# Optimization experiments

Hardware: AMD Instinct MI355X
Metric: run time of the kernel (lower is better)

Reference implementation:

```python
import jax, jax.numpy as jnp
import numpy as np

K = 8           # neighbor_num
H = 8           # n_heads
DH = 64         # dim_single_head


def setup_inputs() -> dict:
    key = jax.random.key(0)
    ks = jax.random.split(key, 6)
    B, N, D = 2, 8192, 256
    inner = H * DH  # 512
    x = jax.random.normal(ks[0], (B, N, D), jnp.float32)
    center_pos3d = jax.random.normal(ks[1], (B, N, 3), jnp.float32)
    Wq = jax.random.normal(ks[2], (D, inner), jnp.float32) * 0.02
    Wkv = jax.random.normal(ks[3], (D, 2 * inner), jnp.float32) * 0.02
    Wout = jax.random.normal(ks[4], (inner, D), jnp.float32) * 0.02
    bout = jnp.zeros((D,), jnp.float32)
    return {"x": x, "center_pos3d": center_pos3d, "Wq": Wq, "Wkv": Wkv,
            "Wout": Wout, "bout": bout}


def _knn_idx(pos, k):
    # pos: [B,N,3] -> indices of k nearest neighbors per point, [B,N,k]
    sq = jnp.sum(pos * pos, axis=-1)                      # [B,N]
    d2 = sq[:, :, None] + sq[:, None, :] - 2.0 * jnp.einsum('bnc,bmc->bnm', pos, pos)
    _, idx = jax.lax.top_k(-d2, k)                        # smallest distances
    return idx


def reference(x, center_pos3d, Wq, Wkv, Wout, bout):
    B, N, D = x.shape
    inner = H * DH
    scale = DH ** -0.5

    idx = _knn_idx(center_pos3d, K)                       # [B,N,K] int32
    # grouping_operation: gather neighbor features -> [B,N,K,D]
    knn_x = jax.vmap(lambda xb, ib: xb[ib])(x, idx)

    q = (x @ Wq).reshape(B, N, H, DH)                     # [B,N,H,DH]
    kv = knn_x @ Wkv                                      # [B,N,K,2*inner]
    k_, v_ = jnp.split(kv, 2, axis=-1)
    k_ = k_.reshape(B, N, K, H, DH)
    v_ = v_.reshape(B, N, K, H, DH)

    dots = jnp.einsum('bnhd,bnkhd->bnhk', q, k_) * scale  # [B,N,H,K]
    attn = jax.nn.softmax(dots, axis=-1)
    out = jnp.einsum('bnhk,bnkhd->bnhd', attn, v_)        # [B,N,H,DH]
    out = out.reshape(B, N, inner)
    return out @ Wout + bout                              # dropout p=0 -> identity
```

## Files before the change

kernel.cpp:

```cpp
#include <hip/hip_runtime.h>
#include <hip/hip_bf16.h>

#define N_PTS 8192
#define KNN 8

typedef __attribute__((ext_vector_type(8))) short short8;
typedef __attribute__((ext_vector_type(4))) float float4v;
typedef unsigned long long u64;

static __device__ __forceinline__ short f2bf(float f) {
    unsigned u = __float_as_uint(f);
    unsigned r = (u + 0x7FFFu + ((u >> 16) & 1u)) >> 16;
    return (short)r;
}
static __device__ __forceinline__ float bf2f(short s) {
    return __uint_as_float(((unsigned)(unsigned short)s) << 16);
}

static __device__ __forceinline__ unsigned sortkey(float f) {
    unsigned u = __float_as_uint(f);
    return u ^ (((unsigned)((int)u >> 31)) | 0x80000000u);
}

static __device__ __forceinline__ void ins8(u64* best, u64 x) {
#pragma unroll
    for (int j = 0; j < 8; ++j) {
        const u64 lo = x < best[j] ? x : best[j];
        const u64 hi = x < best[j] ? best[j] : x;
        best[j] = lo; x = hi;
    }
}

static __device__ __forceinline__ void vmin_acc(float& acc, float d) {
    asm("v_min_f32 %0, %0, %1" : "+v"(acc) : "v"(d));
}
static __device__ __forceinline__ void vsort2(float& a, float& x) {
    float lo, hi;
    asm("v_min_f32 %0, %2, %3\n\tv_max_f32 %1, %2, %3"
        : "=&v"(lo), "=v"(hi) : "v"(a), "v"(x));
    a = lo; x = hi;
}

__global__ __launch_bounds__(256) void fused_knn_conv(const float* __restrict__ pos,
                                                      u64* __restrict__ partial,
                                                      const float* __restrict__ x,
                                                      const float* __restrict__ Wq,
                                                      const float* __restrict__ Wkv,
                                                      const float* __restrict__ Wout,
                                                      short* __restrict__ xb,
                                                      short* __restrict__ wqkvt,
                                                      short* __restrict__ woutt)
{
    __shared__ __align__(16) char smem[16896];
    const int tid = threadIdx.x;
    const int g5 = blockIdx.x / 5;
    const int r5 = blockIdx.x % 5;

    if (r5 == 0) {
        const int kb = g5;
        float4* cand = (float4*)smem;
        unsigned short* buf = (unsigned short*)(smem + 8192);

        const int p   = kb & 15;
        const int qg  = kb >> 4;
        const int batch = qg >> 5;
        const int q_in_b = (qg & 31) * 256 + tid;
        const float* bpos = pos + (long)batch * N_PTS * 3;

        if (tid < 128) {
            const float* src = bpos + (p * 512 + tid * 4) * 3;
            const float4 f0 = *(const float4*)(src);
            const float4 f1 = *(const float4*)(src + 4);
            const float4 f2 = *(const float4*)(src + 8);
            const int c0 = tid * 4;
            cand[c0 + 0] = make_float4(f0.x, f0.y, f0.z,
                                       fmaf(f0.x, f0.x, fmaf(f0.y, f0.y, f0.z * f0.z)));
            cand[c0 + 1] = make_float4(f0.w, f1.x, f1.y,
                                       fmaf(f0.w, f0.w, fmaf(f1.x, f1.x, f1.y * f1.y)));
            cand[c0 + 2] = make_float4(f1.z, f1.w, f2.x,
                                       fmaf(f1.z, f1.z, fmaf(f1.w, f1.w, f2.x * f2.x)));
            cand[c0 + 3] = make_float4(f2.y, f2.z, f2.w,
                                       fmaf(f2.y, f2.y, fmaf(f2.z, f2.z, f2.w * f2.w)));
        }
        __syncthreads();

        const float qx = bpos[q_in_b * 3 + 0];
        const float qy = bpos[q_in_b * 3 + 1];
        const float qz = bpos[q_in_b * 3 + 2];
        const float nqx = -2.0f * qx;
        const float nqy = -2.0f * qy;
        const float nqz = -2.0f * qz;

        float bmin[32];
#pragma unroll
        for (int j = 0; j < 32; ++j) bmin[j] = 3.0e38f;

        for (int base = 0; base < 512; base += 32) {
#pragma unroll
            for (int g = 0; g < 32; ++g) {
                const float4 c = cand[base + g];
                const float d = fmaf(c.x, nqx, fmaf(c.y, nqy, fmaf(c.z, nqz, c.w)));
                vmin_acc(bmin[g], d);
            }
        }

        float t8[8];
#pragma unroll
        for (int j = 0; j < 8; ++j) t8[j] = 3.0e38f;
#pragma unroll
        for (int i = 0; i < 32; ++i) {
            float x_ = bmin[i];
#pragma unroll
            for (int j = 0; j < 8; ++j)
                vsort2(t8[j], x_);
        }
        const float t = t8[7];

        int cnt = 0;
        for (int base = 0; base < 512; base += 32) {
#pragma unroll
            for (int g = 0; g < 32; ++g) {
                const float4 c = cand[base + g];
                const float d = fmaf(c.x, nqx, fmaf(c.y, nqy, fmaf(c.z, nqz, c.w)));
                if (d <= t) {
                    buf[tid * 17 + (cnt < 16 ? cnt : 16)] = (unsigned short)(base + g);
                    ++cnt;
                }
            }
        }

        u64 best[8];
#pragma unroll
        for (int j = 0; j < 8; ++j) best[j] = ~0ULL;

        if (cnt <= 16) {
            for (int u = 0; u < cnt; ++u) {
                const int i = buf[tid * 17 + u];
                const float4 c = cand[i];
                const float d = fmaf(c.x, nqx, fmaf(c.y, nqy, fmaf(c.z, nqz, c.w)));
                ins8(best, ((u64)sortkey(d) << 32) | (unsigned)(p * 512 + i));
            }
        } else {
            for (int i = 0; i < 512; ++i) {
                const float4 c = cand[i];
                const float d = fmaf(c.x, nqx, fmaf(c.y, nqy, fmaf(c.z, nqz, c.w)));
                const u64 x_ = ((u64)sortkey(d) << 32) | (unsigned)(p * 512 + i);
                if (x_ < best[7]) ins8(best, x_);
            }
        }

        const long qglob = (long)batch * N_PTS + q_in_b;
#pragma unroll
        for (int j = 0; j < 8; ++j)
            partial[(long)(p * 8 + j) * 16384 + qglob] = best[j];

    } else {
        const int bid = g5 * 4 + (r5 - 1);
        if (bid < 2048) {
            const int i = bid * 256 + tid;
            const float4 a = ((const float4*)x)[i * 2];
            const float4 b = ((const float4*)x)[i * 2 + 1];
            short8 w = {f2bf(a.x), f2bf(a.y), f2bf(a.z), f2bf(a.w),
                        f2bf(b.x), f2bf(b.y), f2bf(b.z), f2bf(b.w)};
            ((short8*)xb)[i] = w;
        } else if (bid < 2560) {
            const int o = (bid - 2048) * 256 + tid;
            const int n = o >> 8, k = o & 255;
            wqkvt[o] = f2bf(Wq[(long)k * 512 + n]);
        } else if (bid < 3584) {
            const int o = (bid - 2560) * 256 + tid;
            const int n = o >> 8, k = o & 255;
            wqkvt[131072 + o] = f2bf(Wkv[(long)k * 1024 + n]);
        } else {
            const int o = (bid - 3584) * 256 + tid;
            const int n = o >> 9, k = o & 511;
            woutt[o] = f2bf(Wout[(long)k * 256 + n]);
        }
    }
}

__global__ __launch_bounds__(256) void fused_gemm_merge(const short* __restrict__ A,
                                                        const short* __restrict__ Bt,
                                                        short* __restrict__ qall,
                                                        short* __restrict__ kvall,
                                                        const u64* __restrict__ partial,
                                                        int* __restrict__ idxo)
{
    __shared__ short As[128][40];
    __shared__ short Bs[128][40];

    const int tid = threadIdx.x;

    if (blockIdx.x < 64) {
        const int q = blockIdx.x * 256 + tid;
        u64 best[8];
#pragma unroll
        for (int j = 0; j < 8; ++j) best[j] = ~0ULL;
        for (int s = 0; s < 128; ++s) {
            u64 x = partial[(long)s * 16384 + q];
            if (x < best[7]) ins8(best, x);
        }
#pragma unroll
        for (int j = 0; j < 8; ++j)
            idxo[(long)q * 8 + j] = (int)(best[j] & 0xFFFFFFFFu);
        return;
    }

    const int id = blockIdx.x - 64;
    const int bx = id % 12;
    const int by = id / 12;

    const int lane = tid & 63;
    const int wv   = tid >> 6;
    const int quad = lane >> 4;
    const int l15  = lane & 15;
    const int m0 = by * 128;
    const int n0 = bx * 128;
    const int mh = (wv & 1) * 64, nh = (wv >> 1) * 64;

    const int srow  = tid >> 1;
    const int shalf = (tid & 1) * 16;
    const int Kd = 256;

    float4v acc[4][4];
#pragma unroll
    for (int i = 0; i < 4; ++i)
#pragma unroll
        for (int j = 0; j < 4; ++j) acc[i][j] = (float4v)(0.f);

    for (int k0 = 0; k0 < Kd; k0 += 32) {
        const short8* asrc = (const short8*)(A + (long)(m0 + srow) * Kd + k0 + shalf);
        const short8* bsrc = (const short8*)(Bt + (long)(n0 + srow) * Kd + k0 + shalf);
        *(short8*)&As[srow][shalf]     = asrc[0];
        *(short8*)&As[srow][shalf + 8] = asrc[1];
        *(short8*)&Bs[srow][shalf]     = bsrc[0];
        *(short8*)&Bs[srow][shalf + 8] = bsrc[1];
        __syncthreads();

        short8 af[4], bfv[4];
#pragma unroll
        for (int i = 0; i < 4; ++i)
            af[i] = *(const short8*)&As[mh + i * 16 + l15][quad * 8];
#pragma unroll
        for (int j = 0; j < 4; ++j)
            bfv[j] = *(const short8*)&Bs[nh + j * 16 + l15][quad * 8];
#pragma unroll
        for (int i = 0; i < 4; ++i)
#pragma unroll
            for (int j = 0; j < 4; ++j)
                acc[i][j] = __builtin_amdgcn_mfma_f32_16x16x32_bf16(af[i], bfv[j], acc[i][j], 0, 0, 0);
        __syncthreads();
    }

    short* Cb;
    int stride, cb;
    if (n0 < 512) { Cb = qall;  stride = 512;  cb = n0; }
    else          { Cb = kvall; stride = 1024; cb = n0 - 512; }

#pragma unroll
    for (int i = 0; i < 4; ++i)
#pragma unroll
        for (int j = 0; j < 4; ++j) {
            const int col = cb + nh + j * 16 + l15;
#pragma unroll
            for (int r = 0; r < 4; ++r) {
                const int row = m0 + mh + i * 16 + quad * 4 + r;
                Cb[(long)row * stride + col] = f2bf(acc[i][j][r]);
            }
        }
}

__global__ __launch_bounds__(256) void attn_kernel(const short* qall,
                                                   const short* __restrict__ kvall,
                                                   const int* __restrict__ idxp,
                                                   short* outp)
{
    __shared__ float attn_s[4][8][8];
    const int wave = threadIdx.x >> 6;
    const int lane = threadIdx.x & 63;
    const int g = blockIdx.x * 4 + wave;
    const int b = g >> 13;
    const int* myidx = idxp + (long)g * 8;

    {
        const int h = lane >> 3;
        const int k = lane & 7;
        const int j = myidx[k];
        const short8* qrow = (const short8*)(qall + (long)g * 512 + h * 64);
        const short8* krow = (const short8*)(kvall + ((long)(b * N_PTS + j)) * 1024 + h * 64);

        float dot = 0.f;
#pragma unroll
        for (int c = 0; c < 8; ++c) {
            const short8 qv = qrow[c];
            const short8 kv = krow[c];
#pragma unroll
            for (int e = 0; e < 8; ++e)
                dot = fmaf(bf2f(qv[e]), bf2f(kv[e]), dot);
        }
        dot *= 0.125f;

        float m = dot;
#pragma unroll
        for (int off = 1; off < 8; off <<= 1)
            m = fmaxf(m, __shfl_xor(m, off, 8));
        const float e = __expf(dot - m);
        float ssum = e;
#pragma unroll
        for (int off = 1; off < 8; off <<= 1)
            ssum += __shfl_xor(ssum, off, 8);
        attn_s[wave][h][k] = e / ssum;
    }
    __syncthreads();

    const int d8 = lane * 8;
    const int h2 = lane >> 3;
    float o[8] = {0.f, 0.f, 0.f, 0.f, 0.f, 0.f, 0.f, 0.f};
#pragma unroll
    for (int kk = 0; kk < 8; ++kk) {
        const int jj = myidx[kk];
        const float w = attn_s[wave][h2][kk];
        const short8 v = *(const short8*)(kvall + ((long)(b * N_PTS + jj)) * 1024 + 512 + d8);
#pragma unroll
        for (int e = 0; e < 8; ++e)
            o[e] = fmaf(w, bf2f(v[e]), o[e]);
    }
    short8 ov = {f2bf(o[0]), f2bf(o[1]), f2bf(o[2]), f2bf(o[3]),
                 f2bf(o[4]), f2bf(o[5]), f2bf(o[6]), f2bf(o[7])};
    *(short8*)(outp + (long)g * 512 + d8) = ov;
}

__global__ __launch_bounds__(256) void gemm_out(const short* __restrict__ A,
                                                const short* __restrict__ Bt,
                                                const float* __restrict__ bias,
                                                float* __restrict__ C,
                                                int N, int Kd)
{
    __shared__ short As[128][40];
    __shared__ short Bs[128][40];

    const int tid  = threadIdx.x;
    const int lane = tid & 63;
    const int wv   = tid >> 6;
    const int quad = lane >> 4;
    const int l15  = lane & 15;
    const int m0 = blockIdx.y * 128;
    const int n0 = blockIdx.x * 128;
    const int mh = (wv & 1) * 64, nh = (wv >> 1) * 64;

    const int srow  = tid >> 1;
    const int shalf = (tid & 1) * 16;

    float4v acc[4][4];
#pragma unroll
    for (int i = 0; i < 4; ++i)
#pragma unroll
        for (int j = 0; j < 4; ++j) acc[i][j] = (float4v)(0.f);

    for (int k0 = 0; k0 < Kd; k0 += 32) {
        const short8* asrc = (const short8*)(A + (long)(m0 + srow) * Kd + k0 + shalf);
        const short8* bsrc = (const short8*)(Bt + (long)(n0 + srow) * Kd + k0 + shalf);
        *(short8*)&As[srow][shalf]     = asrc[0];
        *(short8*)&As[srow][shalf + 8] = asrc[1];
        *(short8*)&Bs[srow][shalf]     = bsrc[0];
        *(short8*)&Bs[srow][shalf + 8] = bsrc[1];
        __syncthreads();

        short8 af[4], bfv[4];
#pragma unroll
        for (int i = 0; i < 4; ++i)
            af[i] = *(const short8*)&As[mh + i * 16 + l15][quad * 8];
#pragma unroll
        for (int j = 0; j < 4; ++j)
            bfv[j] = *(const short8*)&Bs[nh + j * 16 + l15][quad * 8];
#pragma unroll
        for (int i = 0; i < 4; ++i)
#pragma unroll
            for (int j = 0; j < 4; ++j)
                acc[i][j] = __builtin_amdgcn_mfma_f32_16x16x32_bf16(af[i], bfv[j], acc[i][j], 0, 0, 0);
        __syncthreads();
    }

#pragma unroll
    for (int i = 0; i < 4; ++i)
#pragma unroll
        for (int j = 0; j < 4; ++j) {
            const int col = n0 + nh + j * 16 + l15;
            const float bb = bias[col];
#pragma unroll
            for (int r = 0; r < 4; ++r) {
                const int row = m0 + mh + i * 16 + quad * 4 + r;
                C[(long)row * N + col] = acc[i][j][r] + bb;
            }
        }
}

extern "C" void kernel_launch(void* const* d_in, const int* in_sizes, int n_in,
                              void* d_out, int out_size, void* d_ws, size_t ws_size,
                              hipStream_t stream)
{
    const float* x    = (const float*)d_in[0];
    const float* pos  = (const float*)d_in[1];
    const float* Wq   = (const float*)d_in[2];
    const float* Wkv  = (const float*)d_in[3];
    const float* Wout = (const float*)d_in[4];
    const float* bout = (const float*)d_in[5];
    float* out = (float*)d_out;

    const int M = 16384;

    char* ws = (char*)d_ws;
    int*   idxp  = (int*)ws;                          ws += 1 << 19;
    short* qall  = (short*)ws;                        ws += (long)M * 512 * 2;
    short* kvall = (short*)ws;                        ws += (long)M * 1024 * 2;
    short* xb    = (short*)ws;                        ws += (long)M * 256 * 2;
    short* wqkvt = (short*)ws;                        ws += 1536 * 256 * 2;
    short* woutt = (short*)ws;                        ws += 256 * 512 * 2;
    u64*  partial = (u64*)ws;                         ws += (long)128 * 16384 * 8;

    fused_knn_conv<<<5120, 256, 0, stream>>>(pos, partial, x, Wq, Wkv, Wout,
                                             xb, wqkvt, woutt);
    fused_gemm_merge<<<1600, 256, 0, stream>>>(xb, wqkvt, qall, kvall, partial, idxp);
    attn_kernel<<<M / 4, 256, 0, stream>>>(qall, kvall, idxp, qall);
    gemm_out<<<dim3(2, 128), 256, 0, stream>>>(qall, woutt, bout, out, 256, 512);
}
```

Baseline: 283.0 us.

## Reorder attention queries by Morton-coded spatial cells to improve neighbor-gather locality

```diff
diff --git a/kernel.cpp b/kernel.cpp
--- a/kernel.cpp
+++ b/kernel.cpp
@@ -3,10 +3,15 @@
 
 #define N_PTS 8192
 #define KNN 8
+#define GRID_DIM 32
+#define NCELLS 32768
+#define CELL_S 0.25f
+#define GRID_LO (-4.0f)
 
 typedef __attribute__((ext_vector_type(8))) short short8;
 typedef __attribute__((ext_vector_type(4))) float float4v;
 typedef unsigned long long u64;
+typedef unsigned int u32;
 
 static __device__ __forceinline__ short f2bf(float f) {
     unsigned u = __float_as_uint(f);
@@ -39,6 +44,17 @@
     asm("v_min_f32 %0, %2, %3\n\tv_max_f32 %1, %2, %3"
         : "=&v"(lo), "=v"(hi) : "v"(a), "v"(x));
     a = lo; x = hi;
+}
+
+static __device__ __forceinline__ int cell_coord(float v) {
+    int c = (int)floorf((v - GRID_LO) * (1.0f / CELL_S));
+    c = c < 0 ? 0 : c;
+    c = c > GRID_DIM - 1 ? GRID_DIM - 1 : c;
+    return c;
+}
+static __device__ __forceinline__ unsigned spread5(int v) {
+    return (unsigned)((v & 1) | ((v & 2) << 2) | ((v & 4) << 4)
+                    | ((v & 8) << 6) | ((v & 16) << 8));
 }
 
 __global__ __launch_bounds__(256) void fused_knn_conv(const float* __restrict__ pos,
@@ -49,10 +65,27 @@
                                                       const float* __restrict__ Wout,
                                                       short* __restrict__ xb,
                                                       short* __restrict__ wqkvt,
-                                                      short* __restrict__ woutt)
+                                                      short* __restrict__ woutt,
+                                                      u32* __restrict__ cellCount,
+                                                      unsigned short* __restrict__ cid)
 {
     __shared__ __align__(16) char smem[16896];
     const int tid = threadIdx.x;
+
+    if (blockIdx.x >= 5120) {
+        const int i = (blockIdx.x - 5120) * 256 + tid;
+        const int b = i >> 13;
+        const float px = pos[i * 3 + 0];
+        const float py = pos[i * 3 + 1];
+        const float pz = pos[i * 3 + 2];
+        const unsigned m = spread5(cell_coord(px))
+                         | (spread5(cell_coord(py)) << 1)
+                         | (spread5(cell_coord(pz)) << 2);
+        cid[i] = (unsigned short)m;
+        atomicAdd(&cellCount[b * NCELLS + m], 1u);
+        return;
+    }
+
     const int g5 = blockIdx.x / 5;
     const int r5 = blockIdx.x % 5;
 
@@ -184,12 +217,38 @@
                                                         short* __restrict__ qall,
                                                         short* __restrict__ kvall,
                                                         const u64* __restrict__ partial,
-                                                        int* __restrict__ idxo)
+                                                        int* __restrict__ idxo,
+                                                        const u32* __restrict__ cellCount,
+                                                        u32* __restrict__ cellStart)
 {
     __shared__ short As[128][40];
     __shared__ short Bs[128][40];
 
     const int tid = threadIdx.x;
+
+    if (blockIdx.x >= 1600) {
+        u32* psum = (u32*)As;
+        const int b = blockIdx.x - 1600;
+        const u32* cnt = cellCount + b * NCELLS;
+        u32* st = cellStart + b * (NCELLS + 1);
+
+        u32 sum = 0;
+        for (int j = 0; j < 128; ++j) sum += cnt[tid * 128 + j];
+        psum[tid] = sum;
+        __syncthreads();
+        if (tid == 0) {
+            u32 a = 0;
+            for (int i = 0; i < 256; ++i) { const u32 t = psum[i]; psum[i] = a; a += t; }
+        }
+        __syncthreads();
+        u32 run = psum[tid];
+        for (int j = 0; j < 128; ++j) {
+            st[tid * 128 + j] = run;
+            run += cnt[tid * 128 + j];
+        }
+        if (tid == 255) st[NCELLS] = run;
+        return;
+    }
 
     if (blockIdx.x < 64) {
         const int q = blockIdx.x * 256 + tid;
@@ -270,15 +329,29 @@
         }
 }
 
+__global__ __launch_bounds__(256) void scatter_kernel(const unsigned short* __restrict__ cid,
+                                                      const u32* __restrict__ cellStart,
+                                                      u32* __restrict__ cellOff,
+                                                      int* __restrict__ rowmap)
+{
+    const int i = blockIdx.x * 256 + threadIdx.x;
+    const int b = i >> 13;
+    const int c = cid[i];
+    const u32 dst = cellStart[b * (NCELLS + 1) + c] + atomicAdd(&cellOff[b * NCELLS + c], 1u);
+    rowmap[b * N_PTS + dst] = i;
+}
+
 __global__ __launch_bounds__(256) void attn_kernel(const short* qall,
                                                    const short* __restrict__ kvall,
                                                    const int* __restrict__ idxp,
+                                                   const int* __restrict__ order,
                                                    short* outp)
 {
     __shared__ float attn_s[4][8][8];
     const int wave = threadIdx.x >> 6;
     const int lane = threadIdx.x & 63;
-    const int g = blockIdx.x * 4 + wave;
+    const int sbid = ((blockIdx.x & 7) << 9) | (blockIdx.x >> 3);
+    const int g = order[sbid * 4 + wave];
     const int b = g >> 13;
     const int* myidx = idxp + (long)g * 8;
 
@@ -417,10 +490,19 @@
     short* wqkvt = (short*)ws;                        ws += 1536 * 256 * 2;
     short* woutt = (short*)ws;                        ws += 256 * 512 * 2;
     u64*  partial = (u64*)ws;                         ws += (long)128 * 16384 * 8;
-
-    fused_knn_conv<<<5120, 256, 0, stream>>>(pos, partial, x, Wq, Wkv, Wout,
-                                             xb, wqkvt, woutt);
-    fused_gemm_merge<<<1600, 256, 0, stream>>>(xb, wqkvt, qall, kvall, partial, idxp);
-    attn_kernel<<<M / 4, 256, 0, stream>>>(qall, kvall, idxp, qall);
+    u32*  cellCount = (u32*)ws;                       ws += 2L * NCELLS * 4;
+    u32*  cellOff   = (u32*)ws;                       ws += 2L * NCELLS * 4;
+    u32*  cellStart = (u32*)ws;                       ws += 2L * (NCELLS + 1) * 4 + 56;
+    unsigned short* cid = (unsigned short*)ws;        ws += (long)M * 2;
+    int*   rowmap = (int*)ws;                         ws += (long)M * 4;
+
+    hipMemsetAsync(cellCount, 0, 4L * NCELLS * 4, stream);
+
+    fused_knn_conv<<<5184, 256, 0, stream>>>(pos, partial, x, Wq, Wkv, Wout,
+                                             xb, wqkvt, woutt, cellCount, cid);
+    fused_gemm_merge<<<1602, 256, 0, stream>>>(xb, wqkvt, qall, kvall, partial,
+                                               idxp, cellCount, cellStart);
+    scatter_kernel<<<64, 256, 0, stream>>>(cid, cellStart, cellOff, rowmap);
+    attn_kernel<<<M / 4, 256, 0, stream>>>(qall, kvall, idxp, rowmap, qall);
     gemm_out<<<dim3(2, 128), 256, 0, stream>>>(qall, woutt, bout, out, 256, 512);
 }
```

Result: faster. 266.1 us, median of 2 (-6.0%).
